# Kernel tuning notes

Hardware: AMD Instinct MI355X
Metric: run time of the kernel (lower is better)

## Reference

```python
import jax, jax.numpy as jnp
import numpy as np

H, B, D, C = 6, 512, 2048, 1000   # heads (5 ICs + backbone exit), batch, feat dim, classes
TAU = 0.5                          # confidence_threshold


def setup_inputs() -> dict:
    key = jax.random.key(0)
    k1, k2, k3, k4 = jax.random.split(key, 4)
    feats = jax.random.normal(k1, (H, B, D), dtype=jnp.float32)          # pooled reps at each exit
    W = jax.random.normal(k2, (H, D, C), dtype=jnp.float32) * 0.07       # per-head classifier weights
    b = jax.random.normal(k3, (H, C), dtype=jnp.float32) * 0.1
    y_true = jax.random.randint(k4, (B,), 0, C)
    return {"feats": feats, "W": W, "b": b, "y_true": y_true}


def reference(feats, W, b, y_true):
    # Per-head logits for every sample (vectorized replacement for the shrinking-batch loop).
    logits = jnp.einsum('hbd,hdc->hbc', feats, W) + b[:, None, :]        # [H, B, C]
    logp = jax.nn.log_softmax(logits, axis=-1)
    conf = jnp.exp(logp).max(axis=-1)                                    # [H, B] max softmax prob (prob_conf=True)

    # Early-exit routing: first head with conf >= TAU; else head with max confidence
    # (argmax returns the first occurrence, matching the strict '>' update in find_exit).
    exited = conf >= TAU                                                  # [H, B]
    any_exit = exited.any(axis=0)                                         # [B]
    first_exit = jnp.argmax(exited, axis=0)                               # [B] first True along heads
    best_conf = jnp.argmax(conf, axis=0)                                  # [B] fallback exit
    exit_idx = jnp.where(any_exit, first_exit, best_conf)                 # [B] == sample_exited_at

    # Gather the chosen head's logits per sample (vectorized masked-scatter of sample_outputs).
    outputs = jnp.take_along_axis(logits, exit_idx[None, :, None], axis=0)[0]   # [B, C]

    # criterion_ic: cross-entropy loss + accuracy on routed outputs
    out_logp = jax.nn.log_softmax(outputs, axis=-1)
    loss = -jnp.take_along_axis(out_logp, y_true[:, None], axis=1).mean()
    acc = (outputs.argmax(axis=-1) == y_true).astype(jnp.float32).mean()
    return outputs, exit_idx.astype(jnp.int32), loss, acc
```

## Files before the change

kernel.cpp:

```cpp
#include <hip/hip_runtime.h>
#include <math.h>

#define Hn 6
#define Bn 512
#define Dn 2048
#define Cn 1000
#define TAUv 0.5f
#define KT 32

typedef __attribute__((ext_vector_type(8))) short short8;
typedef __attribute__((ext_vector_type(4))) float f32x4;

union FragU { unsigned d[4]; short8 s; };

__device__ __forceinline__ unsigned pack_hi2(unsigned u0, unsigned u1) {
  return __builtin_amdgcn_perm(u1, u0, 0x07060302u);
}

__device__ __forceinline__ void stage_tile(
    short (*AhB)[128][8], short (*AlB)[128][8],
    short (*BhB)[34], short (*BlB)[34],
    int am, int ac, int bn4, int bk0,
    float4 av0, float4 av1, float4 bv0, float4 bv1)
{
  {
    const float af[8] = {av0.x, av0.y, av0.z, av0.w, av1.x, av1.y, av1.z, av1.w};
    unsigned hi[4], lo[4];
#pragma unroll
    for (int j = 0; j < 4; ++j) {
      const unsigned u0 = __float_as_uint(af[2 * j]);
      const unsigned u1 = __float_as_uint(af[2 * j + 1]);
      const float h0 = __uint_as_float(u0 & 0xFFFF0000u);
      const float h1 = __uint_as_float(u1 & 0xFFFF0000u);
      const unsigned l0 = __float_as_uint(af[2 * j] - h0);
      const unsigned l1 = __float_as_uint(af[2 * j + 1] - h1);
      hi[j] = pack_hi2(u0, u1);
      lo[j] = pack_hi2(l0, l1);
    }
    *(uint4*)(&AhB[ac][am][0]) = make_uint4(hi[0], hi[1], hi[2], hi[3]);
    *(uint4*)(&AlB[ac][am][0]) = make_uint4(lo[0], lo[1], lo[2], lo[3]);
  }
  {
    const float f0[4] = {bv0.x, bv0.y, bv0.z, bv0.w};
    const float f1[4] = {bv1.x, bv1.y, bv1.z, bv1.w};
#pragma unroll
    for (int j = 0; j < 4; ++j) {
      const unsigned u0 = __float_as_uint(f0[j]);
      const unsigned u1 = __float_as_uint(f1[j]);
      const float h0 = __uint_as_float(u0 & 0xFFFF0000u);
      const float h1 = __uint_as_float(u1 & 0xFFFF0000u);
      const unsigned l0 = __float_as_uint(f0[j] - h0);
      const unsigned l1 = __float_as_uint(f1[j] - h1);
      *(unsigned*)(&BhB[bn4 + j][bk0]) = pack_hi2(u0, u1);
      *(unsigned*)(&BlB[bn4 + j][bk0]) = pack_hi2(l0, l1);
    }
  }
}

__global__ __launch_bounds__(512, 1) void gemm_k(
    const float* __restrict__ feats, const float* __restrict__ Wg,
    const float* __restrict__ bias, float* __restrict__ logits)
{
  const int h  = blockIdx.z;
  const int m0 = blockIdx.y * 128;
  const int n0 = blockIdx.x * 128;

  const float* A  = feats + (size_t)h * Bn * Dn;
  const float* Bg = Wg    + (size_t)h * Dn * Cn;

  __shared__ __align__(16) short Ah[2][4][128][8];
  __shared__ __align__(16) short Al[2][4][128][8];
  __shared__ __align__(16) short Bh[2][128][34];
  __shared__ __align__(16) short Bl[2][128][34];

  const int t = threadIdx.x;
  const int am = t >> 2, ac = t & 3;
  const int bn4 = (t & 31) << 2, bk0 = (t >> 5) << 1;

  const int lane = t & 63;
  const int w    = t >> 6;
  const int wm   = (w & 3) * 32;
  const int wn   = (w >> 2) * 64;
  const int fl   = lane & 15;
  const int fq   = lane >> 4;

  f32x4 acc[2][4];
#pragma unroll
  for (int i = 0; i < 2; ++i)
#pragma unroll
    for (int j = 0; j < 4; ++j) acc[i][j] = (f32x4){0.f, 0.f, 0.f, 0.f};

  const float* aptr = A + (size_t)(m0 + am) * Dn + ac * 8;
  const bool bvalid = (n0 + bn4) < Cn;
  const float* bptr = Bg + (size_t)bk0 * Cn + n0 + bn4;

  {
    const float4 av0 = *(const float4*)(aptr);
    const float4 av1 = *(const float4*)(aptr + 4);
    float4 bv0 = make_float4(0.f, 0.f, 0.f, 0.f), bv1 = bv0;
    if (bvalid) {
      bv0 = *(const float4*)(bptr);
      bv1 = *(const float4*)(bptr + Cn);
    }
    stage_tile(Ah[0], Al[0], Bh[0], Bl[0], am, ac, bn4, bk0, av0, av1, bv0, bv1);
  }

  int p = 0;
  for (int kb = 0; kb < Dn; kb += KT) {
    __syncthreads();
    const int kn = kb + KT;
    const bool more = (kn < Dn);

    float4 nav0, nav1, nbv0, nbv1;
    if (more) {
      nav0 = *(const float4*)(aptr + kn);
      nav1 = *(const float4*)(aptr + kn + 4);
      nbv0 = make_float4(0.f, 0.f, 0.f, 0.f); nbv1 = nbv0;
      if (bvalid) {
        nbv0 = *(const float4*)(bptr + (size_t)kn * Cn);
        nbv1 = *(const float4*)(bptr + (size_t)kn * Cn + Cn);
      }
    }

    FragU ah[2], al[2];
#pragma unroll
    for (int mt = 0; mt < 2; ++mt) {
      const int m = wm + mt * 16 + fl;
      ah[mt].s = *(const short8*)(&Ah[p][fq][m][0]);
      al[mt].s = *(const short8*)(&Al[p][fq][m][0]);
    }
#pragma unroll
    for (int nt = 0; nt < 4; ++nt) {
      const int n = wn + nt * 16 + fl;
      FragU bh, bl;
      const unsigned* bhp = (const unsigned*)(&Bh[p][0][0]) + n * 17 + fq * 4;
      const unsigned* blp = (const unsigned*)(&Bl[p][0][0]) + n * 17 + fq * 4;
#pragma unroll
      for (int q = 0; q < 4; ++q) { bh.d[q] = bhp[q]; bl.d[q] = blp[q]; }
#pragma unroll
      for (int mt = 0; mt < 2; ++mt) {
        acc[mt][nt] = __builtin_amdgcn_mfma_f32_16x16x32_bf16(ah[mt].s, bh.s, acc[mt][nt], 0, 0, 0);
        acc[mt][nt] = __builtin_amdgcn_mfma_f32_16x16x32_bf16(ah[mt].s, bl.s, acc[mt][nt], 0, 0, 0);
        acc[mt][nt] = __builtin_amdgcn_mfma_f32_16x16x32_bf16(al[mt].s, bh.s, acc[mt][nt], 0, 0, 0);
      }
    }

    if (more)
      stage_tile(Ah[p ^ 1], Al[p ^ 1], Bh[p ^ 1], Bl[p ^ 1],
                 am, ac, bn4, bk0, nav0, nav1, nbv0, nbv1);
    p ^= 1;
  }

#pragma unroll
  for (int nt = 0; nt < 4; ++nt) {
    const int col = n0 + wn + nt * 16 + fl;
    if (col >= Cn) continue;
    const float bv = bias[(size_t)h * Cn + col];
#pragma unroll
    for (int mt = 0; mt < 2; ++mt) {
      const int rbase = m0 + wm + mt * 16 + fq * 4;
#pragma unroll
      for (int r = 0; r < 4; ++r) {
        logits[((size_t)h * Bn + rbase + r) * Cn + col] = acc[mt][nt][r] + bv;
      }
    }
  }
}

__global__ __launch_bounds__(256) void conf_k(const float* __restrict__ logits,
                                              float* __restrict__ ms,
                                              float* __restrict__ ss,
                                              float* __restrict__ scalars)
{
  if (blockIdx.x == 0 && threadIdx.x == 0) { scalars[0] = 0.f; scalars[1] = 0.f; }
  const int w = threadIdx.x >> 6, lane = threadIdx.x & 63;
  const int r = blockIdx.x * 4 + w;
  const float* row = logits + (size_t)r * Cn;

  float vv[16];
#pragma unroll
  for (int i = 0; i < 4; ++i) {
    const int c4 = i * 256 + lane * 4;
    if (c4 + 3 < Cn) {
      const float4 v = *(const float4*)(row + c4);
      vv[4 * i] = v.x; vv[4 * i + 1] = v.y; vv[4 * i + 2] = v.z; vv[4 * i + 3] = v.w;
    } else {
#pragma unroll
      for (int j = 0; j < 4; ++j)
        vv[4 * i + j] = (c4 + j < Cn) ? row[c4 + j] : -3.4e38f;
    }
  }
  float m = -3.4e38f;
#pragma unroll
  for (int i = 0; i < 16; ++i) m = fmaxf(m, vv[i]);
#pragma unroll
  for (int off = 32; off >= 1; off >>= 1) m = fmaxf(m, __shfl_xor(m, off));
  float s = 0.f;
#pragma unroll
  for (int i = 0; i < 16; ++i) s += (vv[i] > -3.0e38f) ? expf(vv[i] - m) : 0.f;
#pragma unroll
  for (int off = 32; off >= 1; off >>= 1) s += __shfl_xor(s, off);
  if (lane == 0) { ms[r] = m; ss[r] = s; }
}

__global__ __launch_bounds__(256) void pick_k(
    const float* __restrict__ logits, const float* __restrict__ ms,
    const float* __restrict__ ss, const int* __restrict__ y,
    float* __restrict__ out, float* __restrict__ out_exit,
    float* __restrict__ scalars)
{
  const int b = blockIdx.x, t = threadIdx.x;

  int first = -1, best = 0;
  float bestc = -3.4e38f;
#pragma unroll
  for (int h = 0; h < Hn; ++h) {
    const float c = 1.0f / ss[h * Bn + b];
    if (first < 0 && c >= TAUv) first = h;
    if (c > bestc) { bestc = c; best = h; }
  }
  const int ex = (first >= 0) ? first : best;
  const float* row = logits + ((size_t)ex * Bn + b) * Cn;

  const int c4 = t * 4;
  float vv[4] = {-3.4e38f, -3.4e38f, -3.4e38f, -3.4e38f};
  if (c4 + 3 < Cn) {
    const float4 v = *(const float4*)(row + c4);
    vv[0] = v.x; vv[1] = v.y; vv[2] = v.z; vv[3] = v.w;
  } else {
#pragma unroll
    for (int j = 0; j < 4; ++j) if (c4 + j < Cn) vv[j] = row[c4 + j];
  }
  float vm = -3.4e38f; int im = 1 << 30;
#pragma unroll
  for (int j = 0; j < 4; ++j) {
    const int c = c4 + j;
    if (c < Cn) {
      out[(size_t)b * Cn + c] = vv[j];
      if (vv[j] > vm) { vm = vv[j]; im = c; }
    }
  }
  const int lane = t & 63, w = t >> 6;
#pragma unroll
  for (int off = 32; off >= 1; off >>= 1) {
    const float ov = __shfl_xor(vm, off);
    const int   oi = __shfl_xor(im, off);
    if (ov > vm || (ov == vm && oi < im)) { vm = ov; im = oi; }
  }
  __shared__ float rm[4]; __shared__ int ri[4];
  if (lane == 0) { rm[w] = vm; ri[w] = im; }
  __syncthreads();
  if (t == 0) {
    float bm = rm[0]; int bi = ri[0];
    for (int q = 1; q < 4; ++q)
      if (rm[q] > bm || (rm[q] == bm && ri[q] < bi)) { bm = rm[q]; bi = ri[q]; }
    const int yt = y[b];
    const float lp = row[yt] - ms[ex * Bn + b] - logf(ss[ex * Bn + b]);
    out_exit[b] = (float)ex;
    atomicAdd(&scalars[0], -lp * (1.0f / (float)Bn));
    atomicAdd(&scalars[1], ((bi == yt) ? 1.f : 0.f) * (1.0f / (float)Bn));
  }
}

extern "C" void kernel_launch(void* const* d_in, const int* in_sizes, int n_in,
                              void* d_out, int out_size, void* d_ws, size_t ws_size,
                              hipStream_t stream) {
  const float* feats = (const float*)d_in[0];
  const float* W     = (const float*)d_in[1];
  const float* bias  = (const float*)d_in[2];
  const int*   y     = (const int*)d_in[3];
  float* out = (float*)d_out;

  float* logits = (float*)d_ws;
  float* ms     = logits + (size_t)Hn * Bn * Cn;
  float* ss     = ms + Hn * Bn;

  float* out_exit    = out + (size_t)Bn * Cn;
  float* out_scalars = out + (size_t)Bn * Cn + Bn;

  dim3 g1(8, 4, Hn);
  gemm_k<<<g1, 512, 0, stream>>>(feats, W, bias, logits);
  conf_k<<<(Hn * Bn) / 4, 256, 0, stream>>>(logits, ms, ss, out_scalars);
  pick_k<<<Bn, 256, 0, stream>>>(logits, ms, ss, y, out, out_exit, out_scalars);
}
```

Measured before the change: 200.0 us.

## Shrink GEMM tiles to 64x64, deepen prefetch, and restage B into fragment layout

The split-bf16 GEMM moves from 128x128 tiles with 512 threads to 64x64 tiles with 256 threads and launch bounds allowing 4 blocks per CU. The grid grows from 192 to 768 blocks to fill more of the chip's CUs. Global loads are now prefetched two K-steps ahead through register double buffering. The B shared-memory tile is stored in the same chunked [4][64][8] layout as A, so fragments load as one 16-byte read instead of four scalar reads. Smaller tiles reuse less data per load and so raise global traffic, but they give better occupancy and latency hiding.

```diff
diff --git a/kernel.cpp b/kernel.cpp
--- a/kernel.cpp
+++ b/kernel.cpp
@@ -7,6 +7,7 @@
 #define Cn 1000
 #define TAUv 0.5f
 #define KT 32
+#define NITER (Dn / KT)
 
 typedef __attribute__((ext_vector_type(8))) short short8;
 typedef __attribute__((ext_vector_type(4))) float f32x4;
@@ -17,9 +18,24 @@
   return __builtin_amdgcn_perm(u1, u0, 0x07060302u);
 }
 
+typedef short (*TileP)[64][8];
+
+__device__ __forceinline__ void load_tile(const float* aptr, const float* bptr, bool bvalid,
+                                          int kb, float4& av0, float4& av1,
+                                          float4& bv0, float4& bv1)
+{
+  av0 = *(const float4*)(aptr + kb);
+  av1 = *(const float4*)(aptr + kb + 4);
+  bv0 = make_float4(0.f, 0.f, 0.f, 0.f);
+  bv1 = bv0;
+  if (bvalid) {
+    bv0 = *(const float4*)(bptr + (size_t)kb * Cn);
+    bv1 = *(const float4*)(bptr + (size_t)kb * Cn + Cn);
+  }
+}
+
 __device__ __forceinline__ void stage_tile(
-    short (*AhB)[128][8], short (*AlB)[128][8],
-    short (*BhB)[34], short (*BlB)[34],
+    TileP AhB, TileP AlB, TileP BhB, TileP BlB,
     int am, int ac, int bn4, int bk0,
     float4 av0, float4 av1, float4 bv0, float4 bv1)
 {
@@ -43,6 +59,7 @@
   {
     const float f0[4] = {bv0.x, bv0.y, bv0.z, bv0.w};
     const float f1[4] = {bv1.x, bv1.y, bv1.z, bv1.w};
+    const int chunk = bk0 >> 3, dw = (bk0 >> 1) & 3;
 #pragma unroll
     for (int j = 0; j < 4; ++j) {
       const unsigned u0 = __float_as_uint(f0[j]);
@@ -51,108 +68,96 @@
       const float h1 = __uint_as_float(u1 & 0xFFFF0000u);
       const unsigned l0 = __float_as_uint(f0[j] - h0);
       const unsigned l1 = __float_as_uint(f1[j] - h1);
-      *(unsigned*)(&BhB[bn4 + j][bk0]) = pack_hi2(u0, u1);
-      *(unsigned*)(&BlB[bn4 + j][bk0]) = pack_hi2(l0, l1);
-    }
-  }
-}
-
-__global__ __launch_bounds__(512, 1) void gemm_k(
+      ((unsigned*)&BhB[chunk][bn4 + j][0])[dw] = pack_hi2(u0, u1);
+      ((unsigned*)&BlB[chunk][bn4 + j][0])[dw] = pack_hi2(l0, l1);
+    }
+  }
+}
+
+__global__ __launch_bounds__(256, 4) void gemm_k(
     const float* __restrict__ feats, const float* __restrict__ Wg,
     const float* __restrict__ bias, float* __restrict__ logits)
 {
   const int h  = blockIdx.z;
-  const int m0 = blockIdx.y * 128;
-  const int n0 = blockIdx.x * 128;
+  const int m0 = blockIdx.y * 64;
+  const int n0 = blockIdx.x * 64;
 
   const float* A  = feats + (size_t)h * Bn * Dn;
   const float* Bg = Wg    + (size_t)h * Dn * Cn;
 
-  __shared__ __align__(16) short Ah[2][4][128][8];
-  __shared__ __align__(16) short Al[2][4][128][8];
-  __shared__ __align__(16) short Bh[2][128][34];
-  __shared__ __align__(16) short Bl[2][128][34];
+  __shared__ __align__(16) short Ah[2][4][64][8];
+  __shared__ __align__(16) short Al[2][4][64][8];
+  __shared__ __align__(16) short Bh[2][4][64][8];
+  __shared__ __align__(16) short Bl[2][4][64][8];
 
   const int t = threadIdx.x;
   const int am = t >> 2, ac = t & 3;
-  const int bn4 = (t & 31) << 2, bk0 = (t >> 5) << 1;
+  const int bn4 = (t & 15) << 2, bk0 = (t >> 4) << 1;
 
   const int lane = t & 63;
   const int w    = t >> 6;
-  const int wm   = (w & 3) * 32;
-  const int wn   = (w >> 2) * 64;
+  const int wm   = (w & 1) * 32;
+  const int wn   = (w >> 1) * 32;
   const int fl   = lane & 15;
   const int fq   = lane >> 4;
 
-  f32x4 acc[2][4];
+  f32x4 acc[2][2];
 #pragma unroll
   for (int i = 0; i < 2; ++i)
 #pragma unroll
-    for (int j = 0; j < 4; ++j) acc[i][j] = (f32x4){0.f, 0.f, 0.f, 0.f};
+    for (int j = 0; j < 2; ++j) acc[i][j] = (f32x4){0.f, 0.f, 0.f, 0.f};
 
   const float* aptr = A + (size_t)(m0 + am) * Dn + ac * 8;
   const bool bvalid = (n0 + bn4) < Cn;
   const float* bptr = Bg + (size_t)bk0 * Cn + n0 + bn4;
 
-  {
-    const float4 av0 = *(const float4*)(aptr);
-    const float4 av1 = *(const float4*)(aptr + 4);
-    float4 bv0 = make_float4(0.f, 0.f, 0.f, 0.f), bv1 = bv0;
-    if (bvalid) {
-      bv0 = *(const float4*)(bptr);
-      bv1 = *(const float4*)(bptr + Cn);
-    }
-    stage_tile(Ah[0], Al[0], Bh[0], Bl[0], am, ac, bn4, bk0, av0, av1, bv0, bv1);
-  }
-
-  int p = 0;
-  for (int kb = 0; kb < Dn; kb += KT) {
+  float4 a0[2], a1[2], b0[2], b1[2];
+
+  load_tile(aptr, bptr, bvalid, 0,  a0[0], a1[0], b0[0], b1[0]);
+  load_tile(aptr, bptr, bvalid, KT, a0[1], a1[1], b0[1], b1[1]);
+  stage_tile(Ah[0], Al[0], Bh[0], Bl[0], am, ac, bn4, bk0, a0[0], a1[0], b0[0], b1[0]);
+
+#define COMPUTE(pb)                                                                   \
+  {                                                                                   \
+    FragU ah[2], al[2];                                                               \
+    _Pragma("unroll")                                                                 \
+    for (int mt = 0; mt < 2; ++mt) {                                                  \
+      const int m = wm + mt * 16 + fl;                                                \
+      ah[mt].s = *(const short8*)(&Ah[pb][fq][m][0]);                                 \
+      al[mt].s = *(const short8*)(&Al[pb][fq][m][0]);                                 \
+    }                                                                                 \
+    _Pragma("unroll")                                                                 \
+    for (int nt = 0; nt < 2; ++nt) {                                                  \
+      const int n = wn + nt * 16 + fl;                                                \
+      FragU bh, bl;                                                                   \
+      bh.s = *(const short8*)(&Bh[pb][fq][n][0]);                                     \
+      bl.s = *(const short8*)(&Bl[pb][fq][n][0]);                                     \
+      _Pragma("unroll")                                                               \
+      for (int mt = 0; mt < 2; ++mt) {                                                \
+        acc[mt][nt] = __builtin_amdgcn_mfma_f32_16x16x32_bf16(ah[mt].s, bh.s, acc[mt][nt], 0, 0, 0); \
+        acc[mt][nt] = __builtin_amdgcn_mfma_f32_16x16x32_bf16(ah[mt].s, bl.s, acc[mt][nt], 0, 0, 0); \
+        acc[mt][nt] = __builtin_amdgcn_mfma_f32_16x16x32_bf16(al[mt].s, bh.s, acc[mt][nt], 0, 0, 0); \
+      }                                                                               \
+    }                                                                                 \
+  }
+
+  for (int it = 0; it < NITER; it += 2) {
     __syncthreads();
-    const int kn = kb + KT;
-    const bool more = (kn < Dn);
-
-    float4 nav0, nav1, nbv0, nbv1;
-    if (more) {
-      nav0 = *(const float4*)(aptr + kn);
-      nav1 = *(const float4*)(aptr + kn + 4);
-      nbv0 = make_float4(0.f, 0.f, 0.f, 0.f); nbv1 = nbv0;
-      if (bvalid) {
-        nbv0 = *(const float4*)(bptr + (size_t)kn * Cn);
-        nbv1 = *(const float4*)(bptr + (size_t)kn * Cn + Cn);
-      }
-    }
-
-    FragU ah[2], al[2];
-#pragma unroll
-    for (int mt = 0; mt < 2; ++mt) {
-      const int m = wm + mt * 16 + fl;
-      ah[mt].s = *(const short8*)(&Ah[p][fq][m][0]);
-      al[mt].s = *(const short8*)(&Al[p][fq][m][0]);
-    }
-#pragma unroll
-    for (int nt = 0; nt < 4; ++nt) {
-      const int n = wn + nt * 16 + fl;
-      FragU bh, bl;
-      const unsigned* bhp = (const unsigned*)(&Bh[p][0][0]) + n * 17 + fq * 4;
-      const unsigned* blp = (const unsigned*)(&Bl[p][0][0]) + n * 17 + fq * 4;
-#pragma unroll
-      for (int q = 0; q < 4; ++q) { bh.d[q] = bhp[q]; bl.d[q] = blp[q]; }
-#pragma unroll
-      for (int mt = 0; mt < 2; ++mt) {
-        acc[mt][nt] = __builtin_amdgcn_mfma_f32_16x16x32_bf16(ah[mt].s, bh.s, acc[mt][nt], 0, 0, 0);
-        acc[mt][nt] = __builtin_amdgcn_mfma_f32_16x16x32_bf16(ah[mt].s, bl.s, acc[mt][nt], 0, 0, 0);
-        acc[mt][nt] = __builtin_amdgcn_mfma_f32_16x16x32_bf16(al[mt].s, bh.s, acc[mt][nt], 0, 0, 0);
-      }
-    }
-
-    if (more)
-      stage_tile(Ah[p ^ 1], Al[p ^ 1], Bh[p ^ 1], Bl[p ^ 1],
-                 am, ac, bn4, bk0, nav0, nav1, nbv0, nbv1);
-    p ^= 1;
-  }
-
-#pragma unroll
-  for (int nt = 0; nt < 4; ++nt) {
+    if (it + 2 < NITER)
+      load_tile(aptr, bptr, bvalid, (it + 2) * KT, a0[0], a1[0], b0[0], b1[0]);
+    COMPUTE(0);
+    stage_tile(Ah[1], Al[1], Bh[1], Bl[1], am, ac, bn4, bk0, a0[1], a1[1], b0[1], b1[1]);
+
+    __syncthreads();
+    if (it + 3 < NITER)
+      load_tile(aptr, bptr, bvalid, (it + 3) * KT, a0[1], a1[1], b0[1], b1[1]);
+    COMPUTE(1);
+    if (it + 2 < NITER)
+      stage_tile(Ah[0], Al[0], Bh[0], Bl[0], am, ac, bn4, bk0, a0[0], a1[0], b0[0], b1[0]);
+  }
+
+#pragma unroll
+  for (int nt = 0; nt < 2; ++nt) {
     const int col = n0 + wn + nt * 16 + fl;
     if (col >= Cn) continue;
     const float bv = bias[(size_t)h * Cn + col];
@@ -278,8 +283,8 @@
   float* out_exit    = out + (size_t)Bn * Cn;
   float* out_scalars = out + (size_t)Bn * Cn + Bn;
 
-  dim3 g1(8, 4, Hn);
-  gemm_k<<<g1, 512, 0, stream>>>(feats, W, bias, logits);
+  dim3 g1(16, 8, Hn);
+  gemm_k<<<g1, 256, 0, stream>>>(feats, W, bias, logits);
   conf_k<<<(Hn * Bn) / 4, 256, 0, stream>>>(logits, ms, ss, out_scalars);
   pick_k<<<Bn, 256, 0, stream>>>(logits, ms, ss, y, out, out_exit, out_scalars);
 }
```

After: 202.7 us. Within noise of the previous version (+1.4%).

## Pre-split inputs to bf16 hi/lo, split-K GEMM with LDS DMA loads

Applied to the files above, without the earlier changes.

Adds separate pre-pass kernels that convert feats and a transposed, padded W into bf16 hi/lo planes using round-to-nearest. The GEMM then streams these planes straight into LDS with global_load_lds, uses a 4x4 MFMA tile per wave on 256 threads, and splits K four ways with atomicAdd into a zeroed logits buffer. This removes per-tile fp32 conversion and transposition from the GEMM loop and raises the block count for occupancy. In exchange it adds extra global traffic for the converted copies, a memset, atomics, and a GEMM loop with no double buffering and two barriers per iteration.

```diff
diff --git a/kernel.cpp b/kernel.cpp
--- a/kernel.cpp
+++ b/kernel.cpp
@@ -5,164 +5,177 @@
 #define Bn 512
 #define Dn 2048
 #define Cn 1000
+#define Cpad 1024
 #define TAUv 0.5f
+#define KSPLIT 4
+#define KPER (Dn / KSPLIT)
 #define KT 32
-
+#define NIT (KPER / KT)
+
+typedef unsigned int u32;
+typedef unsigned short u16;
 typedef __attribute__((ext_vector_type(8))) short short8;
 typedef __attribute__((ext_vector_type(4))) float f32x4;
 
-union FragU { unsigned d[4]; short8 s; };
-
-__device__ __forceinline__ unsigned pack_hi2(unsigned u0, unsigned u1) {
-  return __builtin_amdgcn_perm(u1, u0, 0x07060302u);
-}
-
-__device__ __forceinline__ void stage_tile(
-    short (*AhB)[128][8], short (*AlB)[128][8],
-    short (*BhB)[34], short (*BlB)[34],
-    int am, int ac, int bn4, int bk0,
-    float4 av0, float4 av1, float4 bv0, float4 bv1)
-{
-  {
-    const float af[8] = {av0.x, av0.y, av0.z, av0.w, av1.x, av1.y, av1.z, av1.w};
-    unsigned hi[4], lo[4];
-#pragma unroll
-    for (int j = 0; j < 4; ++j) {
-      const unsigned u0 = __float_as_uint(af[2 * j]);
-      const unsigned u1 = __float_as_uint(af[2 * j + 1]);
-      const float h0 = __uint_as_float(u0 & 0xFFFF0000u);
-      const float h1 = __uint_as_float(u1 & 0xFFFF0000u);
-      const unsigned l0 = __float_as_uint(af[2 * j] - h0);
-      const unsigned l1 = __float_as_uint(af[2 * j + 1] - h1);
-      hi[j] = pack_hi2(u0, u1);
-      lo[j] = pack_hi2(l0, l1);
-    }
-    *(uint4*)(&AhB[ac][am][0]) = make_uint4(hi[0], hi[1], hi[2], hi[3]);
-    *(uint4*)(&AlB[ac][am][0]) = make_uint4(lo[0], lo[1], lo[2], lo[3]);
-  }
-  {
-    const float f0[4] = {bv0.x, bv0.y, bv0.z, bv0.w};
-    const float f1[4] = {bv1.x, bv1.y, bv1.z, bv1.w};
-#pragma unroll
-    for (int j = 0; j < 4; ++j) {
-      const unsigned u0 = __float_as_uint(f0[j]);
-      const unsigned u1 = __float_as_uint(f1[j]);
-      const float h0 = __uint_as_float(u0 & 0xFFFF0000u);
-      const float h1 = __uint_as_float(u1 & 0xFFFF0000u);
-      const unsigned l0 = __float_as_uint(f0[j] - h0);
-      const unsigned l1 = __float_as_uint(f1[j] - h1);
-      *(unsigned*)(&BhB[bn4 + j][bk0]) = pack_hi2(u0, u1);
-      *(unsigned*)(&BlB[bn4 + j][bk0]) = pack_hi2(l0, l1);
-    }
-  }
-}
-
-__global__ __launch_bounds__(512, 1) void gemm_k(
-    const float* __restrict__ feats, const float* __restrict__ Wg,
+union FragU { u32 d[4]; short8 s; };
+
+__device__ __forceinline__ u32 bf16_rne(float f) {
+  const u32 u = __float_as_uint(f);
+  return (u + 0x7FFFu + ((u >> 16) & 1u)) >> 16;
+}
+__device__ __forceinline__ u32 pack_rne2(float f0, float f1, float& r0, float& r1) {
+  const u32 b0 = bf16_rne(f0), b1 = bf16_rne(f1);
+  r0 = f0 - __uint_as_float(b0 << 16);
+  r1 = f1 - __uint_as_float(b1 << 16);
+  return b0 | (b1 << 16);
+}
+
+__device__ __forceinline__ void dma16(const void* g, void* l) {
+  __builtin_amdgcn_global_load_lds(
+      (const __attribute__((address_space(1))) u32*)g,
+      (__attribute__((address_space(3))) u32*)l, 16, 0, 0);
+}
+
+__global__ __launch_bounds__(256) void aconv_k(const float* __restrict__ feats,
+                                               u16* __restrict__ Ah, u16* __restrict__ Al)
+{
+  const size_t i4 = (size_t)blockIdx.x * 256 + threadIdx.x;
+  const float4 v = ((const float4*)feats)[i4];
+  float r0, r1, r2, r3, d0, d1, d2, d3;
+  const u32 h0 = pack_rne2(v.x, v.y, r0, r1);
+  const u32 h1 = pack_rne2(v.z, v.w, r2, r3);
+  const u32 l0 = pack_rne2(r0, r1, d0, d1);
+  const u32 l1 = pack_rne2(r2, r3, d2, d3);
+  ((uint2*)Ah)[i4] = make_uint2(h0, h1);
+  ((uint2*)Al)[i4] = make_uint2(l0, l1);
+}
+
+__global__ __launch_bounds__(256) void bconv_k(const float* __restrict__ W,
+                                               u16* __restrict__ Bh, u16* __restrict__ Bl)
+{
+  const int h  = blockIdx.z;
+  const int d0 = blockIdx.x * 64;
+  const int n0 = blockIdx.y * 64;
+  __shared__ float tile[64][65];
+  const int t = threadIdx.x;
+
+#pragma unroll
+  for (int rr = 0; rr < 4; ++rr) {
+    const int d  = rr * 16 + (t >> 4);
+    const int n4 = (t & 15) * 4;
+    const float* src = W + ((size_t)h * Dn + d0 + d) * Cn;
+    float4 v = make_float4(0.f, 0.f, 0.f, 0.f);
+    const int ng = n0 + n4;
+    if (ng + 3 < Cn) {
+      v = *(const float4*)(src + ng);
+    } else {
+      if (ng + 0 < Cn) v.x = src[ng + 0];
+      if (ng + 1 < Cn) v.y = src[ng + 1];
+      if (ng + 2 < Cn) v.z = src[ng + 2];
+      if (ng + 3 < Cn) v.w = src[ng + 3];
+    }
+    tile[d][n4 + 0] = v.x; tile[d][n4 + 1] = v.y;
+    tile[d][n4 + 2] = v.z; tile[d][n4 + 3] = v.w;
+  }
+  __syncthreads();
+
+#pragma unroll
+  for (int rr = 0; rr < 4; ++rr) {
+    const int nl = rr * 16 + (t >> 4);
+    const int d4 = (t & 15) * 4;
+    const float f0 = tile[d4 + 0][nl], f1 = tile[d4 + 1][nl];
+    const float f2 = tile[d4 + 2][nl], f3 = tile[d4 + 3][nl];
+    float r0, r1, r2, r3, q0, q1, q2, q3;
+    const u32 h0 = pack_rne2(f0, f1, r0, r1);
+    const u32 h1 = pack_rne2(f2, f3, r2, r3);
+    const u32 l0 = pack_rne2(r0, r1, q0, q1);
+    const u32 l1 = pack_rne2(r2, r3, q2, q3);
+    const size_t idx = ((size_t)h * Cpad + n0 + nl) * Dn + d0 + d4;
+    *(uint2*)(Bh + idx) = make_uint2(h0, h1);
+    *(uint2*)(Bl + idx) = make_uint2(l0, l1);
+  }
+}
+
+__global__ __launch_bounds__(256, 3) void gemm_k(
+    const u16* __restrict__ AhG, const u16* __restrict__ AlG,
+    const u16* __restrict__ BhG, const u16* __restrict__ BlG,
     const float* __restrict__ bias, float* __restrict__ logits)
 {
-  const int h  = blockIdx.z;
+  const int h  = blockIdx.z / KSPLIT;
+  const int kz = blockIdx.z % KSPLIT;
   const int m0 = blockIdx.y * 128;
   const int n0 = blockIdx.x * 128;
-
-  const float* A  = feats + (size_t)h * Bn * Dn;
-  const float* Bg = Wg    + (size_t)h * Dn * Cn;
-
-  __shared__ __align__(16) short Ah[2][4][128][8];
-  __shared__ __align__(16) short Al[2][4][128][8];
-  __shared__ __align__(16) short Bh[2][128][34];
-  __shared__ __align__(16) short Bl[2][128][34];
+  const int kbase = kz * KPER;
+
+  __shared__ __align__(16) short Ah[4][128][8];
+  __shared__ __align__(16) short Al[4][128][8];
+  __shared__ __align__(16) short Bh[4][128][8];
+  __shared__ __align__(16) short Bl[4][128][8];
 
   const int t = threadIdx.x;
-  const int am = t >> 2, ac = t & 3;
-  const int bn4 = (t & 31) << 2, bk0 = (t >> 5) << 1;
-
   const int lane = t & 63;
   const int w    = t >> 6;
-  const int wm   = (w & 3) * 32;
-  const int wn   = (w >> 2) * 64;
+  const int wm   = (w & 1) * 64;
+  const int wn   = (w >> 1) * 64;
   const int fl   = lane & 15;
   const int fq   = lane >> 4;
 
-  f32x4 acc[2][4];
-#pragma unroll
-  for (int i = 0; i < 2; ++i)
+  const u16* gmat = (w == 0) ? AhG : (w == 1) ? AlG : (w == 2) ? BhG : BlG;
+  const size_t rowbase = (w < 2) ? ((size_t)h * Bn + m0) : ((size_t)h * Cpad + n0);
+  short* lbase = (w == 0) ? &Ah[0][0][0] : (w == 1) ? &Al[0][0][0]
+               : (w == 2) ? &Bh[0][0][0] : &Bl[0][0][0];
+  const u16* grow = gmat + (rowbase + lane) * (size_t)Dn + kbase;
+  const u16* grow64 = grow + (size_t)64 * Dn;
+
+  f32x4 acc[4][4];
+#pragma unroll
+  for (int i = 0; i < 4; ++i)
 #pragma unroll
     for (int j = 0; j < 4; ++j) acc[i][j] = (f32x4){0.f, 0.f, 0.f, 0.f};
 
-  const float* aptr = A + (size_t)(m0 + am) * Dn + ac * 8;
-  const bool bvalid = (n0 + bn4) < Cn;
-  const float* bptr = Bg + (size_t)bk0 * Cn + n0 + bn4;
-
-  {
-    const float4 av0 = *(const float4*)(aptr);
-    const float4 av1 = *(const float4*)(aptr + 4);
-    float4 bv0 = make_float4(0.f, 0.f, 0.f, 0.f), bv1 = bv0;
-    if (bvalid) {
-      bv0 = *(const float4*)(bptr);
-      bv1 = *(const float4*)(bptr + Cn);
-    }
-    stage_tile(Ah[0], Al[0], Bh[0], Bl[0], am, ac, bn4, bk0, av0, av1, bv0, bv1);
-  }
-
-  int p = 0;
-  for (int kb = 0; kb < Dn; kb += KT) {
+  for (int it = 0; it < NIT; ++it) {
+    const int kk = it * KT;
+#pragma unroll
+    for (int c = 0; c < 4; ++c) {
+      dma16(grow   + kk + c * 8, lbase + c * 1024);
+      dma16(grow64 + kk + c * 8, lbase + c * 1024 + 512);
+    }
     __syncthreads();
-    const int kn = kb + KT;
-    const bool more = (kn < Dn);
-
-    float4 nav0, nav1, nbv0, nbv1;
-    if (more) {
-      nav0 = *(const float4*)(aptr + kn);
-      nav1 = *(const float4*)(aptr + kn + 4);
-      nbv0 = make_float4(0.f, 0.f, 0.f, 0.f); nbv1 = nbv0;
-      if (bvalid) {
-        nbv0 = *(const float4*)(bptr + (size_t)kn * Cn);
-        nbv1 = *(const float4*)(bptr + (size_t)kn * Cn + Cn);
-      }
-    }
-
-    FragU ah[2], al[2];
-#pragma unroll
-    for (int mt = 0; mt < 2; ++mt) {
+
+    FragU ah[4], al[4];
+#pragma unroll
+    for (int mt = 0; mt < 4; ++mt) {
       const int m = wm + mt * 16 + fl;
-      ah[mt].s = *(const short8*)(&Ah[p][fq][m][0]);
-      al[mt].s = *(const short8*)(&Al[p][fq][m][0]);
+      ah[mt].s = *(const short8*)(&Ah[fq][m][0]);
+      al[mt].s = *(const short8*)(&Al[fq][m][0]);
     }
 #pragma unroll
     for (int nt = 0; nt < 4; ++nt) {
       const int n = wn + nt * 16 + fl;
       FragU bh, bl;
-      const unsigned* bhp = (const unsigned*)(&Bh[p][0][0]) + n * 17 + fq * 4;
-      const unsigned* blp = (const unsigned*)(&Bl[p][0][0]) + n * 17 + fq * 4;
-#pragma unroll
-      for (int q = 0; q < 4; ++q) { bh.d[q] = bhp[q]; bl.d[q] = blp[q]; }
-#pragma unroll
-      for (int mt = 0; mt < 2; ++mt) {
+      bh.s = *(const short8*)(&Bh[fq][n][0]);
+      bl.s = *(const short8*)(&Bl[fq][n][0]);
+#pragma unroll
+      for (int mt = 0; mt < 4; ++mt) {
         acc[mt][nt] = __builtin_amdgcn_mfma_f32_16x16x32_bf16(ah[mt].s, bh.s, acc[mt][nt], 0, 0, 0);
         acc[mt][nt] = __builtin_amdgcn_mfma_f32_16x16x32_bf16(ah[mt].s, bl.s, acc[mt][nt], 0, 0, 0);
         acc[mt][nt] = __builtin_amdgcn_mfma_f32_16x16x32_bf16(al[mt].s, bh.s, acc[mt][nt], 0, 0, 0);
       }
     }
-
-    if (more)
-      stage_tile(Ah[p ^ 1], Al[p ^ 1], Bh[p ^ 1], Bl[p ^ 1],
-                 am, ac, bn4, bk0, nav0, nav1, nbv0, nbv1);
-    p ^= 1;
+    __syncthreads();
   }
 
 #pragma unroll
   for (int nt = 0; nt < 4; ++nt) {
     const int col = n0 + wn + nt * 16 + fl;
     if (col >= Cn) continue;
-    const float bv = bias[(size_t)h * Cn + col];
-#pragma unroll
-    for (int mt = 0; mt < 2; ++mt) {
+    const float bv = (kz == 0) ? bias[(size_t)h * Cn + col] : 0.f;
+#pragma unroll
+    for (int mt = 0; mt < 4; ++mt) {
       const int rbase = m0 + wm + mt * 16 + fq * 4;
 #pragma unroll
-      for (int r = 0; r < 4; ++r) {
-        logits[((size_t)h * Bn + rbase + r) * Cn + col] = acc[mt][nt][r] + bv;
-      }
+      for (int r = 0; r < 4; ++r)
+        atomicAdd(&logits[((size_t)h * Bn + rbase + r) * Cn + col], acc[mt][nt][r] + bv);
     }
   }
 }
@@ -274,12 +287,19 @@
   float* logits = (float*)d_ws;
   float* ms     = logits + (size_t)Hn * Bn * Cn;
   float* ss     = ms + Hn * Bn;
+  u16*   AhG    = (u16*)(ss + Hn * Bn);
+  u16*   AlG    = AhG + (size_t)Hn * Bn * Dn;
+  u16*   BhG    = AlG + (size_t)Hn * Bn * Dn;
+  u16*   BlG    = BhG + (size_t)Hn * Cpad * Dn;
 
   float* out_exit    = out + (size_t)Bn * Cn;
   float* out_scalars = out + (size_t)Bn * Cn + Bn;
 
-  dim3 g1(8, 4, Hn);
-  gemm_k<<<g1, 512, 0, stream>>>(feats, W, bias, logits);
+  hipMemsetAsync(logits, 0, (size_t)Hn * Bn * Cn * sizeof(float), stream);
+  aconv_k<<<(Hn * Bn * Dn / 4) / 256, 256, 0, stream>>>(feats, AhG, AlG);
+  bconv_k<<<dim3(Dn / 64, Cpad / 64, Hn), 256, 0, stream>>>(W, BhG, BlG);
+  gemm_k<<<dim3(Cpad / 128, Bn / 128, Hn * KSPLIT), 256, 0, stream>>>(
+      AhG, AlG, BhG, BlG, bias, logits);
   conf_k<<<(Hn * Bn) / 4, 256, 0, stream>>>(logits, ms, ss, out_scalars);
   pick_k<<<Bn, 256, 0, stream>>>(logits, ms, ss, y, out, out_exit, out_scalars);
 }
```

Result: slower. 281.4 us (+40.7%).
